# Kernel tuning notes

Measured on AMD Instinct MI355X. Metric: run time of the kernel, lower is better.

## Reference

```python
import jax, jax.numpy as jnp
import numpy as np

B, C, H, W = 8, 512, 128, 128
CQ = C // 8  # query/key channels
GAMMA = 1.0


def setup_inputs() -> dict:
    key = jax.random.key(0)
    ks = jax.random.split(key, 4)
    return {
        "x": jax.random.normal(ks[0], (B, C, H, W), jnp.float32),
        "Wq": jax.random.normal(ks[1], (C, CQ), jnp.float32) * 0.05,
        "bq": jnp.zeros((CQ,), jnp.float32),
        "Wk": jax.random.normal(ks[2], (C, CQ), jnp.float32) * 0.05,
        "bk": jnp.zeros((CQ,), jnp.float32),
        "Wv": jax.random.normal(ks[3], (C, C), jnp.float32) * 0.05,
        "bv": jnp.zeros((C,), jnp.float32),
    }


def reference(x, Wq, bq, Wk, bk, Wv, bv):
    # 1x1 convs (channels_first) == per-pixel channel matmuls
    q = jnp.einsum('bchw,cd->bdhw', x, Wq) + bq[None, :, None, None]  # (B,CQ,H,W)
    k = jnp.einsum('bchw,cd->bdhw', x, Wk) + bk[None, :, None, None]  # (B,CQ,H,W)
    v = jnp.einsum('bchw,cd->bdhw', x, Wv) + bv[None, :, None, None]  # (B,C,H,W)

    h = x.shape[2]
    # -inf on the h==g diagonal of the vertical (column) attention, as in INF()
    diag_mask = jnp.where(jnp.eye(h, dtype=bool), -jnp.inf, 0.0)  # (H,H)

    # column attention: each (h,w) attends over all rows g in its column w
    energy_H = jnp.einsum('bchw,bcgw->bhwg', q, k) + diag_mask[None, :, None, :]  # (B,H,W,H)
    # row attention: each (h,w) attends over all cols v' in its row h
    energy_W = jnp.einsum('bchw,bchv->bhwv', q, k)  # (B,H,W,W)

    # joint softmax over concatenated H+W logits
    att = jax.nn.softmax(jnp.concatenate([energy_H, energy_W], axis=-1), axis=-1)
    a_H, a_W = att[..., :h], att[..., h:]

    out_H = jnp.einsum('bhwg,bcgw->bchw', a_H, v)
    out_W = jnp.einsum('bhwv,bchv->bchw', a_W, v)
    return GAMMA * (out_H + out_W) + x
```

## Files before the change

### kernel.cpp

```cpp
#include <hip/hip_runtime.h>


#define Bn 8
#define Cn 512
#define CQn 64
#define Hn 128
#define Wn 128
#define HWn (Hn*Wn)
#define GAMMA_F 1.0f

typedef __attribute__((ext_vector_type(8))) short short8;
typedef __attribute__((ext_vector_type(4))) float f32x4;
typedef unsigned short u16;
typedef unsigned int u32;

__device__ __forceinline__ float b2f(u16 h) {
    union { u32 u; float f; } v; v.u = ((u32)h) << 16; return v.f;
}
__device__ __forceinline__ u16 f2b(float f) {
    union { float f; u32 u; } v; v.f = f;
    u32 u = v.u;
    return (u16)((u + 0x7fffu + ((u >> 16) & 1u)) >> 16);
}

#define MFMA(acc, a, b) acc = __builtin_amdgcn_mfma_f32_16x16x32_bf16(a, b, acc, 0, 0, 0)

__global__ __launch_bounds__(256) void k0_wt(const float* __restrict__ wq,
                                             const float* __restrict__ wk,
                                             const float* __restrict__ wv,
                                             u16* __restrict__ wqkh, u16* __restrict__ wqkl,
                                             u16* __restrict__ wvt) {
    int idx = blockIdx.x * 256 + threadIdx.x;
    if (idx >= 128 * 512 + 512 * 512) return;
    if (idx < 128 * 512) {
        int m = idx >> 9, c = idx & 511;
        float v = (m < 64) ? wq[c * 64 + m] : wk[c * 64 + (m - 64)];
        u16 hi = f2b(v);
        wqkh[idx] = hi;
        wqkl[idx] = f2b(v - b2f(hi));
    } else {
        int j = idx - 128 * 512;
        int m = j >> 9, c = j & 511;
        wvt[j] = f2b(wv[c * 512 + m]);
    }
}

__global__ __launch_bounds__(256) void k1_qk(
    const float* __restrict__ x, const u16* __restrict__ wqkh, const u16* __restrict__ wqkl,
    const float* __restrict__ bq, const float* __restrict__ bk,
    u16* __restrict__ qh, u16* __restrict__ ql, u16* __restrict__ kh, u16* __restrict__ kl,
    u16* __restrict__ xh)
{
    __shared__ u16 Ahi[128 * 72];
    __shared__ u16 Alo[128 * 72];
    __shared__ u16 Bhi[128 * 72];
    __shared__ u16 Blo[128 * 72];
    int bid = blockIdx.x;
    int b = bid >> 7, h = bid & 127;
    int t = threadIdx.x;
    int lane = t & 63, wid = t >> 6;
    int quad = lane >> 4, l16 = lane & 15;
    int mw = (wid >> 1) * 64, nw = (wid & 1) * 64;

    f32x4 acc[4][4];
#pragma unroll
    for (int i = 0; i < 4; i++)
#pragma unroll
        for (int j = 0; j < 4; j++) acc[i][j] = (f32x4){0.f, 0.f, 0.f, 0.f};

    const float* xb = x + (size_t)b * Cn * HWn + (size_t)h * 128;
    u16* xhb = xh + ((size_t)(b * Hn + h)) * Wn * Cn;

    for (int ks = 0; ks < 8; ks++) {
        int c0 = ks * 64;
#pragma unroll
        for (int i = 0; i < 4; i++) {
            int chunk = i * 256 + t;
            int m = chunk >> 3, kq = chunk & 7;
            *(short8*)&Ahi[m * 72 + kq * 8] = *(const short8*)(wqkh + (size_t)m * 512 + c0 + kq * 8);
            *(short8*)&Alo[m * 72 + kq * 8] = *(const short8*)(wqkl + (size_t)m * 512 + c0 + kq * 8);
        }
#pragma unroll
        for (int i = 0; i < 4; i++) {
            int chunk = i * 256 + t;
            int kk = chunk >> 4, m = chunk & 15, n8 = m << 3;
            const float* src = xb + (size_t)(c0 + kk) * HWn + n8;
            float4 d0 = *(const float4*)(src);
            float4 d1 = *(const float4*)(src + 4);
            float f[8] = {d0.x, d0.y, d0.z, d0.w, d1.x, d1.y, d1.z, d1.w};
            int col = kk ^ ((m & 7) << 3);
#pragma unroll
            for (int j = 0; j < 8; j++) {
                u16 hi = f2b(f[j]);
                Bhi[(n8 + j) * 72 + col] = hi;
                Blo[(n8 + j) * 72 + col] = f2b(f[j] - b2f(hi));
            }
        }
        __syncthreads();
#pragma unroll
        for (int k2 = 0; k2 < 64; k2 += 32) {
            short8 afh[4], afl[4], bfh[4], bfl[4];
#pragma unroll
            for (int mi = 0; mi < 4; mi++) {
                afh[mi] = *(const short8*)&Ahi[(mw + mi * 16 + l16) * 72 + k2 + quad * 8];
                afl[mi] = *(const short8*)&Alo[(mw + mi * 16 + l16) * 72 + k2 + quad * 8];
            }
#pragma unroll
            for (int ni = 0; ni < 4; ni++) {
                int wrow = nw + ni * 16 + l16;
                int col = (k2 + quad * 8) ^ (((wrow >> 3) & 7) << 3);
                bfh[ni] = *(const short8*)&Bhi[wrow * 72 + col];
                bfl[ni] = *(const short8*)&Blo[wrow * 72 + col];
            }
#pragma unroll
            for (int mi = 0; mi < 4; mi++)
#pragma unroll
                for (int ni = 0; ni < 4; ni++) {
                    MFMA(acc[mi][ni], afh[mi], bfh[ni]);
                    MFMA(acc[mi][ni], afh[mi], bfl[ni]);
                    MFMA(acc[mi][ni], afl[mi], bfh[ni]);
                }
        }
#pragma unroll
        for (int p = 0; p < 4; p++) {
            int w = p * 32 + (t >> 3), kq = t & 7;
            int col = (kq * 8) ^ (((w >> 3) & 7) << 3);
            *(short8*)(xhb + (size_t)w * Cn + c0 + kq * 8) = *(const short8*)&Bhi[w * 72 + col];
        }
        __syncthreads();
    }

#pragma unroll
    for (int mi = 0; mi < 4; mi++) {
        int gm = mw + mi * 16 + quad * 4;
        float bias[4];
#pragma unroll
        for (int r = 0; r < 4; r++) {
            int g = gm + r;
            bias[r] = (g < 64) ? bq[g] : bk[g - 64];
        }
#pragma unroll
        for (int ni = 0; ni < 4; ni++) {
            int w = nw + ni * 16 + l16;
            u16 oh_[4], ol_[4];
#pragma unroll
            for (int r = 0; r < 4; r++) {
                float val = acc[mi][ni][r] + bias[r];
                oh_[r] = f2b(val);
                ol_[r] = f2b(val - b2f(oh_[r]));
            }
            uint2 ph, pl;
            ph.x = (u32)oh_[0] | ((u32)oh_[1] << 16);
            ph.y = (u32)oh_[2] | ((u32)oh_[3] << 16);
            pl.x = (u32)ol_[0] | ((u32)ol_[1] << 16);
            pl.y = (u32)ol_[2] | ((u32)ol_[3] << 16);
            size_t base = ((size_t)((b * Hn + h) * Wn + w)) * CQn;
            if (gm < 64) {
                *(uint2*)(qh + base + gm) = ph;
                *(uint2*)(ql + base + gm) = pl;
            } else {
                *(uint2*)(kh + base + gm - 64) = ph;
                *(uint2*)(kl + base + gm - 64) = pl;
            }
        }
    }
}

__global__ __launch_bounds__(256) void k1_v(
    const u16* __restrict__ xh, const u16* __restrict__ wvt,
    const float* __restrict__ bv, u16* __restrict__ vt)
{
    __shared__ u16 Al[128 * 72];
    __shared__ u16 Bl[128 * 72];
    int bid = blockIdx.x;
    int b = bid / 512;
    int rem = bid % 512;
    int mt = rem >> 7, h = rem & 127;
    int t = threadIdx.x;
    int lane = t & 63, wid = t >> 6;
    int quad = lane >> 4, l16 = lane & 15;
    int mw = (wid >> 1) * 64, nw = (wid & 1) * 64;

    f32x4 acc[4][4];
#pragma unroll
    for (int i = 0; i < 4; i++)
#pragma unroll
        for (int j = 0; j < 4; j++) acc[i][j] = (f32x4){0.f, 0.f, 0.f, 0.f};

    const u16* xhb = xh + ((size_t)(b * Hn + h)) * Wn * Cn;
    const u16* wtm = wvt + (size_t)(mt * 128) * 512;

    for (int ks = 0; ks < 8; ks++) {
        int c0 = ks * 64;
#pragma unroll
        for (int i = 0; i < 4; i++) {
            int chunk = i * 256 + t;
            int m = chunk >> 3, kq = chunk & 7;
            *(short8*)&Al[m * 72 + kq * 8] = *(const short8*)(wtm + (size_t)m * 512 + c0 + kq * 8);
        }
#pragma unroll
        for (int i = 0; i < 4; i++) {
            int chunk = i * 256 + t;
            int w = chunk >> 3, kq = chunk & 7;
            *(short8*)&Bl[w * 72 + kq * 8] = *(const short8*)(xhb + (size_t)w * Cn + c0 + kq * 8);
        }
        __syncthreads();
#pragma unroll
        for (int k2 = 0; k2 < 64; k2 += 32) {
            short8 af[4], bf[4];
#pragma unroll
            for (int mi = 0; mi < 4; mi++)
                af[mi] = *(const short8*)&Al[(mw + mi * 16 + l16) * 72 + k2 + quad * 8];
#pragma unroll
            for (int ni = 0; ni < 4; ni++)
                bf[ni] = *(const short8*)&Bl[(nw + ni * 16 + l16) * 72 + k2 + quad * 8];
#pragma unroll
            for (int mi = 0; mi < 4; mi++)
#pragma unroll
                for (int ni = 0; ni < 4; ni++) MFMA(acc[mi][ni], af[mi], bf[ni]);
        }
        __syncthreads();
    }

#pragma unroll
    for (int mi = 0; mi < 4; mi++) {
        int gm = mt * 128 + mw + mi * 16 + quad * 4;
        float bias[4];
#pragma unroll
        for (int r = 0; r < 4; r++) bias[r] = bv[gm + r];
#pragma unroll
        for (int ni = 0; ni < 4; ni++) {
            int w = nw + ni * 16 + l16;
            u16 o[4];
#pragma unroll
            for (int r = 0; r < 4; r++) o[r] = f2b(acc[mi][ni][r] + bias[r]);
            uint2 p;
            p.x = (u32)o[0] | ((u32)o[1] << 16);
            p.y = (u32)o[2] | ((u32)o[3] << 16);
            *(uint2*)(vt + ((size_t)((b * Wn + w) * Hn + h)) * Cn + gm) = p;
        }
    }
}

__global__ __launch_bounds__(256) void k2_ew(
    const u16* __restrict__ qh, const u16* __restrict__ ql,
    const u16* __restrict__ kh, const u16* __restrict__ kl, float* __restrict__ ew)
{
    __shared__ u16 Akh[128 * 72];
    __shared__ u16 Akl[128 * 72];
    __shared__ u16 Bqh[128 * 72];
    __shared__ u16 Bql[128 * 72];
    int bid = blockIdx.x;
    int b = bid >> 7, h = bid & 127;
    int t = threadIdx.x;
    int lane = t & 63, wid = t >> 6;
    int quad = lane >> 4, l16 = lane & 15;
    int mw = (wid >> 1) * 64, nw = (wid & 1) * 64;

    size_t rowbase = ((size_t)(b * Hn + h)) * Wn * CQn;
#pragma unroll
    for (int i = 0; i < 4; i++) {
        int chunk = i * 256 + t;
        int row = chunk >> 3, kq = chunk & 7;
        size_t off = rowbase + row * 64 + kq * 8;
        *(short8*)&Akh[row * 72 + kq * 8] = *(const short8*)&kh[off];
        *(short8*)&Akl[row * 72 + kq * 8] = *(const short8*)&kl[off];
        *(short8*)&Bqh[row * 72 + kq * 8] = *(const short8*)&qh[off];
        *(short8*)&Bql[row * 72 + kq * 8] = *(const short8*)&ql[off];
    }
    __syncthreads();

    f32x4 acc[4][4];
#pragma unroll
    for (int i = 0; i < 4; i++)
#pragma unroll
        for (int j = 0; j < 4; j++) acc[i][j] = (f32x4){0.f, 0.f, 0.f, 0.f};
#pragma unroll
    for (int k2 = 0; k2 < 64; k2 += 32) {
        short8 afh[4], afl[4], bfh[4], bfl[4];
#pragma unroll
        for (int mi = 0; mi < 4; mi++) {
            afh[mi] = *(const short8*)&Akh[(mw + mi * 16 + l16) * 72 + k2 + quad * 8];
            afl[mi] = *(const short8*)&Akl[(mw + mi * 16 + l16) * 72 + k2 + quad * 8];
        }
#pragma unroll
        for (int ni = 0; ni < 4; ni++) {
            bfh[ni] = *(const short8*)&Bqh[(nw + ni * 16 + l16) * 72 + k2 + quad * 8];
            bfl[ni] = *(const short8*)&Bql[(nw + ni * 16 + l16) * 72 + k2 + quad * 8];
        }
#pragma unroll
        for (int mi = 0; mi < 4; mi++)
#pragma unroll
            for (int ni = 0; ni < 4; ni++) {
                MFMA(acc[mi][ni], afh[mi], bfh[ni]);
                MFMA(acc[mi][ni], afh[mi], bfl[ni]);
                MFMA(acc[mi][ni], afl[mi], bfh[ni]);
            }
    }
#pragma unroll
    for (int mi = 0; mi < 4; mi++) {
        int v0 = mw + mi * 16 + quad * 4;
#pragma unroll
        for (int ni = 0; ni < 4; ni++) {
            int w = nw + ni * 16 + l16;
            *(f32x4*)(ew + ((size_t)((b * Wn + w) * Hn + h)) * Wn + v0) = acc[mi][ni];
        }
    }
}

__global__ __launch_bounds__(256) void k3a_soft(
    const u16* __restrict__ qh, const u16* __restrict__ ql,
    const u16* __restrict__ kh, const u16* __restrict__ kl,
    const float* __restrict__ ew, u16* __restrict__ aH, u16* __restrict__ aW)
{
    __shared__ char smem[73728];
    u16* Akh = (u16*)smem;
    u16* Akl = (u16*)(smem + 18432);
    u16* Bqh = (u16*)(smem + 36864);
    u16* Bql = (u16*)(smem + 55296);
    float* el = (float*)smem;

    int bid = blockIdx.x;
    int b = bid >> 7, w = bid & 127;
    int t = threadIdx.x;
    int lane = t & 63, wid = t >> 6;
    int quad = lane >> 4, l16 = lane & 15;
    int mw = (wid >> 1) * 64, nw = (wid & 1) * 64;

#pragma unroll
    for (int i = 0; i < 4; i++) {
        int chunk = i * 256 + t;
        int row = chunk >> 3, kq = chunk & 7;
        size_t off = ((size_t)((b * Hn + row) * Wn + w)) * CQn + kq * 8;
        *(short8*)&Akh[row * 72 + kq * 8] = *(const short8*)&kh[off];
        *(short8*)&Akl[row * 72 + kq * 8] = *(const short8*)&kl[off];
        *(short8*)&Bqh[row * 72 + kq * 8] = *(const short8*)&qh[off];
        *(short8*)&Bql[row * 72 + kq * 8] = *(const short8*)&ql[off];
    }
    __syncthreads();

    f32x4 acc[4][4];
#pragma unroll
    for (int i = 0; i < 4; i++)
#pragma unroll
        for (int j = 0; j < 4; j++) acc[i][j] = (f32x4){0.f, 0.f, 0.f, 0.f};
#pragma unroll
    for (int k2 = 0; k2 < 64; k2 += 32) {
        short8 afh[4], afl[4], bfh[4], bfl[4];
#pragma unroll
        for (int mi = 0; mi < 4; mi++) {
            afh[mi] = *(const short8*)&Akh[(mw + mi * 16 + l16) * 72 + k2 + quad * 8];
            afl[mi] = *(const short8*)&Akl[(mw + mi * 16 + l16) * 72 + k2 + quad * 8];
        }
#pragma unroll
        for (int ni = 0; ni < 4; ni++) {
            bfh[ni] = *(const short8*)&Bqh[(nw + ni * 16 + l16) * 72 + k2 + quad * 8];
            bfl[ni] = *(const short8*)&Bql[(nw + ni * 16 + l16) * 72 + k2 + quad * 8];
        }
#pragma unroll
        for (int mi = 0; mi < 4; mi++)
#pragma unroll
            for (int ni = 0; ni < 4; ni++) {
                MFMA(acc[mi][ni], afh[mi], bfh[ni]);
                MFMA(acc[mi][ni], afh[mi], bfl[ni]);
                MFMA(acc[mi][ni], afl[mi], bfh[ni]);
            }
    }
    __syncthreads();

#pragma unroll
    for (int mi = 0; mi < 4; mi++) {
        int g0 = mw + mi * 16 + quad * 4;
#pragma unroll
        for (int ni = 0; ni < 4; ni++) {
            int h_ = nw + ni * 16 + l16;
            f32x4 vv = acc[mi][ni];
#pragma unroll
            for (int r = 0; r < 4; r++)
                if (g0 + r == h_) vv[r] = -INFINITY;
            *(f32x4*)&el[h_ * 132 + g0] = vv;
        }
    }
    __syncthreads();

    int h2 = t >> 1, half = t & 1;
    const float* ewr = ew + (((size_t)(b * Wn + w)) * Hn + h2) * Wn + half * 64;
    const float* ehr = &el[h2 * 132 + half * 64];
    f32x4 ew4[16], eh4[16];
#pragma unroll
    for (int i = 0; i < 16; i++) ew4[i] = *(const f32x4*)&ewr[i * 4];
#pragma unroll
    for (int i = 0; i < 16; i++) eh4[i] = *(const f32x4*)&ehr[i * 4];

    float mx = -INFINITY;
#pragma unroll
    for (int i = 0; i < 16; i++)
#pragma unroll
        for (int r = 0; r < 4; r++) {
            mx = fmaxf(mx, eh4[i][r]);
            mx = fmaxf(mx, ew4[i][r]);
        }
    mx = fmaxf(mx, __shfl_xor(mx, 1, 64));

    float s = 0.f;
#pragma unroll
    for (int i = 0; i < 16; i++)
#pragma unroll
        for (int r = 0; r < 4; r++) {
            float e1 = __expf(eh4[i][r] - mx); eh4[i][r] = e1; s += e1;
            float e2 = __expf(ew4[i][r] - mx); ew4[i][r] = e2; s += e2;
        }
    s += __shfl_xor(s, 1, 64);
    float inv = 1.f / s;

    u16* aHr = aH + (((size_t)(b * Wn + w)) * Hn + h2) * Hn + half * 64;
    u16* aWr = aW + (((size_t)(b * Hn + h2)) * Wn + w) * Wn + half * 64;
#pragma unroll
    for (int i = 0; i < 16; i++) {
        uint2 p, q2;
        p.x  = (u32)f2b(eh4[i][0] * inv) | ((u32)f2b(eh4[i][1] * inv) << 16);
        p.y  = (u32)f2b(eh4[i][2] * inv) | ((u32)f2b(eh4[i][3] * inv) << 16);
        q2.x = (u32)f2b(ew4[i][0] * inv) | ((u32)f2b(ew4[i][1] * inv) << 16);
        q2.y = (u32)f2b(ew4[i][2] * inv) | ((u32)f2b(ew4[i][3] * inv) << 16);
        *(uint2*)&aHr[i * 4] = p;
        *(uint2*)&aWr[i * 4] = q2;
    }
}

__global__ __launch_bounds__(256) void k3b_outh(
    const u16* __restrict__ vt, const u16* __restrict__ aH, u16* __restrict__ oh)
{
    __shared__ u16 Al[128 * 136];
    __shared__ u16 Bl[128 * 136];
    int bid = blockIdx.x;
    int ct = bid & 3, w = (bid >> 2) & 127, b = bid >> 9;
    int t = threadIdx.x;
    int lane = t & 63, wid = t >> 6;
    int quad = lane >> 4, l16 = lane & 15;
    int mw = (wid >> 1) * 64, nw = (wid & 1) * 64;

    const u16* vtb = vt + ((size_t)(b * Wn + w)) * Hn * Cn;
    const u16* aHb = aH + ((size_t)(b * Wn + w)) * Hn * Hn;
#pragma unroll
    for (int i = 0; i < 8; i++) {
        int chunk = i * 256 + t;
        int g = chunk >> 4, c8 = (chunk & 15) << 3;
        short8 d = *(const short8*)(vtb + (size_t)g * Cn + ct * 128 + c8);
        u16* dp = (u16*)&d;
        int gs = g ^ ((chunk & 15) << 3);
#pragma unroll
        for (int j = 0; j < 8; j++) Al[(c8 + j) * 136 + gs] = dp[j];
    }
#pragma unroll
    for (int i = 0; i < 8; i++) {
        int chunk = i * 256 + t;
        int h_ = chunk >> 4, g8 = (chunk & 15) << 3;
        *(short8*)&Bl[h_ * 136 + g8] = *(const short8*)(aHb + (size_t)h_ * Hn + g8);
    }
    __syncthreads();

    f32x4 acc[4][4];
#pragma unroll
    for (int i = 0; i < 4; i++)
#pragma unroll
        for (int j = 0; j < 4; j++) acc[i][j] = (f32x4){0.f, 0.f, 0.f, 0.f};
#pragma unroll
    for (int kk = 0; kk < 128; kk += 32) {
        short8 af[4], bf[4];
#pragma unroll
        for (int mi = 0; mi < 4; mi++) {
            int row = mw + mi * 16 + l16;
            int col = (kk + quad * 8) ^ (((row >> 3) & 15) << 3);
            af[mi] = *(const short8*)&Al[row * 136 + col];
        }
#pragma unroll
        for (int ni = 0; ni < 4; ni++)
            bf[ni] = *(const short8*)&Bl[(nw + ni * 16 + l16) * 136 + kk + quad * 8];
#pragma unroll
        for (int mi = 0; mi < 4; mi++)
#pragma unroll
            for (int ni = 0; ni < 4; ni++) MFMA(acc[mi][ni], af[mi], bf[ni]);
    }

#pragma unroll
    for (int mi = 0; mi < 4; mi++) {
        int c0 = mw + mi * 16 + quad * 4;
#pragma unroll
        for (int ni = 0; ni < 4; ni++) {
            int h_ = nw + ni * 16 + l16;
            u16 o[4];
#pragma unroll
            for (int r = 0; r < 4; r++) o[r] = f2b(acc[mi][ni][r]);
            uint2 p;
            p.x = (u32)o[0] | ((u32)o[1] << 16);
            p.y = (u32)o[2] | ((u32)o[3] << 16);
            *(uint2*)(oh + ((size_t)(b * Wn + w) * Hn + h_) * Cn + ct * 128 + c0) = p;
        }
    }
}

__global__ __launch_bounds__(256) void k4_final(
    const u16* __restrict__ vt, const u16* __restrict__ aW,
    const u16* __restrict__ oh, const float* __restrict__ x, float* __restrict__ out)
{
    __shared__ u16 Al[128 * 136];
    __shared__ u16 Bl[128 * 136];
    int bid = blockIdx.x;
    int ct = bid & 3, h = (bid >> 2) & 127, b = bid >> 9;
    int t = threadIdx.x;
    int lane = t & 63, wid = t >> 6;
    int quad = lane >> 4, l16 = lane & 15;
    int mw = (wid >> 1) * 64, nw = (wid & 1) * 64;

    const u16* aWb = aW + ((size_t)(b * Hn + h)) * Wn * Wn;
#pragma unroll
    for (int i = 0; i < 8; i++) {
        int chunk = i * 256 + t;
        int vv = chunk >> 4, c8 = (chunk & 15) << 3;
        short8 d = *(const short8*)(vt + ((size_t)(b * Wn + vv) * Hn + h) * Cn + ct * 128 + c8);
        u16* dp = (u16*)&d;
        int vs = vv ^ ((chunk & 15) << 3);
#pragma unroll
        for (int j = 0; j < 8; j++) Al[(c8 + j) * 136 + vs] = dp[j];
    }
#pragma unroll
    for (int i = 0; i < 8; i++) {
        int chunk = i * 256 + t;
        int w_ = chunk >> 4, v8 = (chunk & 15) << 3;
        *(short8*)&Bl[w_ * 136 + v8] = *(const short8*)(aWb + (size_t)w_ * Wn + v8);
    }
    __syncthreads();

    f32x4 acc[4][4];
#pragma unroll
    for (int i = 0; i < 4; i++)
#pragma unroll
        for (int j = 0; j < 4; j++) acc[i][j] = (f32x4){0.f, 0.f, 0.f, 0.f};
#pragma unroll
    for (int kk = 0; kk < 128; kk += 32) {
        short8 af[4], bf[4];
#pragma unroll
        for (int mi = 0; mi < 4; mi++) {
            int row = mw + mi * 16 + l16;
            int col = (kk + quad * 8) ^ (((row >> 3) & 15) << 3);
            af[mi] = *(const short8*)&Al[row * 136 + col];
        }
#pragma unroll
        for (int ni = 0; ni < 4; ni++)
            bf[ni] = *(const short8*)&Bl[(nw + ni * 16 + l16) * 136 + kk + quad * 8];
#pragma unroll
        for (int mi = 0; mi < 4; mi++)
#pragma unroll
            for (int ni = 0; ni < 4; ni++) MFMA(acc[mi][ni], af[mi], bf[ni]);
    }

#pragma unroll
    for (int mi = 0; mi < 4; mi++) {
        int c0 = mw + mi * 16 + quad * 4;
        int cg = ct * 128 + c0;
#pragma unroll
        for (int ni = 0; ni < 4; ni++) {
            int w_ = nw + ni * 16 + l16;
            uint2 ohp = *(const uint2*)(oh + ((size_t)(b * Wn + w_) * Hn + h) * Cn + cg);
            u16* ohs = (u16*)&ohp;
#pragma unroll
            for (int r = 0; r < 4; r++) {
                size_t xi = (((size_t)(b * Cn + cg + r)) * Hn + h) * Wn + w_;
                out[xi] = GAMMA_F * (acc[mi][ni][r] + b2f(ohs[r])) + x[xi];
            }
        }
    }
}

extern "C" void kernel_launch(void* const* d_in, const int* in_sizes, int n_in,
                              void* d_out, int out_size, void* d_ws, size_t ws_size,
                              hipStream_t stream) {
    const float* x  = (const float*)d_in[0];
    const float* wq = (const float*)d_in[1];
    const float* bq = (const float*)d_in[2];
    const float* wk = (const float*)d_in[3];
    const float* bk = (const float*)d_in[4];
    const float* wv = (const float*)d_in[5];
    const float* bv = (const float*)d_in[6];
    float* out = (float*)d_out;
    char* ws = (char*)d_ws;

    u16*  vt   = (u16*)(ws + 0);
    u16*  qh   = (u16*)(ws + 134217728);
    u16*  ql   = (u16*)(ws + 150994944);
    u16*  kh   = (u16*)(ws + 167772160);
    u16*  kl   = (u16*)(ws + 184549376);
    float* ew  = (float*)(ws + 201326592);
    u16*  wqkh = (u16*)(ws + 201326592);
    u16*  wqkl = (u16*)(ws + 201326592 + 131072);
    u16*  wvt  = (u16*)(ws + 201326592 + 262144);
    u16*  aH   = (u16*)(ws + 268435456);
    u16*  aW   = (u16*)(ws + 301989888);
    u16*  oh   = (u16*)(ws + 134217728);
    u16*  xh   = (u16*)d_out;

    k0_wt<<<dim3(1280), dim3(256), 0, stream>>>(wq, wk, wv, wqkh, wqkl, wvt);
    k1_qk<<<dim3(Bn * 128), dim3(256), 0, stream>>>(x, wqkh, wqkl, bq, bk, qh, ql, kh, kl, xh);
    k1_v<<<dim3(Bn * 512), dim3(256), 0, stream>>>(xh, wvt, bv, vt);
    k2_ew<<<dim3(Bn * Hn), dim3(256), 0, stream>>>(qh, ql, kh, kl, ew);
    k3a_soft<<<dim3(Bn * Wn), dim3(256), 0, stream>>>(qh, ql, kh, kl, ew, aH, aW);
    k3b_outh<<<dim3(Bn * Wn * 4), dim3(256), 0, stream>>>(vt, aH, oh);
    k4_final<<<dim3(Bn * Hn * 4), dim3(256), 0, stream>>>(vt, aW, oh, x, out);
}
```

Before: 920.4 us.

## Stage epilogue outputs through LDS for coalesced global stores and loads

The column-attention output kernel now writes its bf16 tile to shared memory first, then stores 16-byte chunks contiguously to global memory. The final kernel loads the oh tile with coalesced short8 reads into an XOR-swizzled transposed LDS buffer. It then stages the fp32 accumulators through LDS in two halves, so x and out are accessed as float4 along W. This replaces scattered 8-byte and 4-byte strided global accesses, at the cost of extra barriers and LDS traffic.

After: 898.3 us. -2.4%, faster.

```diff
diff --git a/kernel.cpp b/kernel.cpp
--- a/kernel.cpp
+++ b/kernel.cpp
@@ -481,7 +481,9 @@
 #pragma unroll
             for (int ni = 0; ni < 4; ni++) MFMA(acc[mi][ni], af[mi], bf[ni]);
     }
-
+    __syncthreads();
+
+    u16* ot = Al;
 #pragma unroll
     for (int mi = 0; mi < 4; mi++) {
         int c0 = mw + mi * 16 + quad * 4;
@@ -494,8 +496,17 @@
             uint2 p;
             p.x = (u32)o[0] | ((u32)o[1] << 16);
             p.y = (u32)o[2] | ((u32)o[3] << 16);
-            *(uint2*)(oh + ((size_t)(b * Wn + w) * Hn + h_) * Cn + ct * 128 + c0) = p;
-        }
+            *(uint2*)&ot[h_ * 136 + c0] = p;
+        }
+    }
+    __syncthreads();
+
+    u16* ohb = oh + ((size_t)(b * Wn + w)) * Hn * Cn + ct * 128;
+#pragma unroll
+    for (int i = 0; i < 8; i++) {
+        int chunk = i * 256 + t;
+        int h_ = chunk >> 4, c8 = (chunk & 15) << 3;
+        *(short8*)(ohb + (size_t)h_ * Cn + c8) = *(const short8*)&ot[h_ * 136 + c8];
     }
 }
 
@@ -553,21 +564,56 @@
 #pragma unroll
             for (int ni = 0; ni < 4; ni++) MFMA(acc[mi][ni], af[mi], bf[ni]);
     }
-
-#pragma unroll
-    for (int mi = 0; mi < 4; mi++) {
-        int c0 = mw + mi * 16 + quad * 4;
-        int cg = ct * 128 + c0;
-#pragma unroll
-        for (int ni = 0; ni < 4; ni++) {
-            int w_ = nw + ni * 16 + l16;
-            uint2 ohp = *(const uint2*)(oh + ((size_t)(b * Wn + w_) * Hn + h) * Cn + cg);
-            u16* ohs = (u16*)&ohp;
-#pragma unroll
-            for (int r = 0; r < 4; r++) {
-                size_t xi = (((size_t)(b * Cn + cg + r)) * Hn + h) * Wn + w_;
-                out[xi] = GAMMA_F * (acc[mi][ni][r] + b2f(ohs[r])) + x[xi];
-            }
+    __syncthreads();
+
+    u16* ohT = Al;
+    const u16* ohb = oh + ((size_t)b * Wn) * Hn * Cn + (size_t)h * Cn + ct * 128;
+#pragma unroll
+    for (int i = 0; i < 8; i++) {
+        int chunk = i * 256 + t;
+        int w_ = chunk >> 4, c8 = (chunk & 15) << 3;
+        short8 d = *(const short8*)(ohb + (size_t)w_ * (Hn * Cn) + c8);
+        u16* dp = (u16*)&d;
+        int ws = w_ ^ ((chunk & 15) << 3);
+#pragma unroll
+        for (int j = 0; j < 8; j++) ohT[(c8 + j) * 136 + ws] = dp[j];
+    }
+
+    float* el = (float*)Bl;
+
+#pragma unroll
+    for (int p = 0; p < 2; p++) {
+        __syncthreads();
+        if ((mw >> 6) == p) {
+#pragma unroll
+            for (int mi = 0; mi < 4; mi++) {
+                int c0 = (mw & 63) + mi * 16 + quad * 4;
+#pragma unroll
+                for (int ni = 0; ni < 4; ni++) {
+                    int w_ = nw + ni * 16 + l16;
+#pragma unroll
+                    for (int r = 0; r < 4; r++) el[(c0 + r) * 132 + w_] = acc[mi][ni][r];
+                }
+            }
+        }
+        __syncthreads();
+#pragma unroll
+        for (int rep = 0; rep < 8; rep++) {
+            int crl = rep * 8 + (t >> 5);
+            int cr  = p * 64 + crl;
+            int w0  = (t & 31) * 4;
+            f32x4 ev = *(const f32x4*)&el[crl * 132 + w0];
+            int s = ((cr >> 3) & 15) << 3;
+            uint2 op = *(const uint2*)&ohT[cr * 136 + (w0 ^ s)];
+            u16* ohs = (u16*)&op;
+            size_t gx = ((size_t)(b * Cn + ct * 128 + cr)) * HWn + (size_t)h * Wn + w0;
+            float4 xv = *(const float4*)(x + gx);
+            float4 ov;
+            ov.x = GAMMA_F * (ev[0] + b2f(ohs[0])) + xv.x;
+            ov.y = GAMMA_F * (ev[1] + b2f(ohs[1])) + xv.y;
+            ov.z = GAMMA_F * (ev[2] + b2f(ohs[2])) + xv.z;
+            ov.w = GAMMA_F * (ev[3] + b2f(ohs[3])) + xv.w;
+            *(float4*)(out + gx) = ov;
         }
     }
 }
```
